# Kernel optimization log

Hardware: AMD Instinct MI355X
Metric: run time of the kernel (lower is better)

The kernel has to match this reference:

```python
import jax, jax.numpy as jnp
import numpy as np

N = 200000
C = 128
VOX = 0.05
EPS = 1e-5
OFFSETS = np.array([[dz, dy, dx] for dz in (-1, 0, 1) for dy in (-1, 0, 1) for dx in (-1, 0, 1)], dtype=np.int64)


def setup_inputs() -> dict:
    key = jax.random.key(0)
    ks = jax.random.split(key, 8)
    gp = jax.random.normal(ks[0], (N, 14), jnp.float32)
    # ---- voxelization tables (int constants, computed once in numpy) ----
    pts = np.asarray(gp[:, :3], dtype=np.float64)
    vc = np.floor(pts / VOX).astype(np.int64)
    vc = vc - vc.min(axis=0)
    mx = vc.max(axis=0) + 1
    h = vc[:, 0] * mx[1] * mx[2] + vc[:, 1] * mx[2] + vc[:, 2]
    uh, inv = np.unique(h, return_inverse=True)
    M = int(uh.shape[0])
    vcoord = np.zeros((M, 3), np.int64)
    vcoord[inv] = vc  # coords identical for same hash
    nbr_idx = np.zeros((M, 27), np.int32)
    nbr_mask = np.zeros((M, 27), np.float32)
    for o in range(27):
        nc = vcoord + OFFSETS[o]
        inb = (nc >= 0).all(1) & (nc < mx).all(1)
        nh = nc[:, 0] * mx[1] * mx[2] + nc[:, 1] * mx[2] + nc[:, 2]
        pos = np.clip(np.searchsorted(uh, nh), 0, M - 1)
        found = inb & (uh[pos] == nh)
        nbr_idx[:, o] = np.where(found, pos, 0)
        nbr_mask[:, o] = found.astype(np.float32)
    s = 0.05
    return {
        'gaussian_params': gp,
        'w_enc': jax.random.normal(ks[1], (14, C), jnp.float32) * s,
        'b_enc': jnp.zeros((C,), jnp.float32),
        'ln_g': jnp.ones((C,), jnp.float32),
        'ln_b': jnp.zeros((C,), jnp.float32),
        'conv_w': jax.random.normal(ks[2], (4, 27, C, C), jnp.float32) * s,
        'bn_g': jnp.ones((4, C), jnp.float32),
        'bn_b': jnp.zeros((4, C), jnp.float32),
        'w1': jax.random.normal(ks[3], (C, C // 2), jnp.float32) * s,
        'b1': jnp.zeros((C // 2,), jnp.float32),
        'w2': jax.random.normal(ks[4], (C // 2, 14), jnp.float32) * s,
        'b2': jnp.zeros((14,), jnp.float32),
        'nbr_mask': jnp.asarray(nbr_mask),
        'inv_idx': jnp.asarray(inv.astype(np.int32)),
        'nbr_idx': jnp.asarray(nbr_idx),
        'num_voxels': M,
    }


def _bn(x, g, b):
    m = x.mean(0)
    v = x.var(0)
    return (x - m) * jax.lax.rsqrt(v + EPS) * g + b


def _subm(x, W, nbr_idx, nbr_mask):
    # submanifold 3x3x3 conv: sum over 27 offsets of masked neighbor gather @ W[o]
    out = jnp.zeros_like(x)
    for o in range(27):
        out = out + (x[nbr_idx[:, o]] * nbr_mask[:, o:o + 1]) @ W[o]
    return out


def _forward(gp, w_enc, b_enc, ln_g, ln_b, conv_w, bn_g, bn_b, w1, b1, w2, b2, nbr_mask, inv_idx, nbr_idx, num_voxels):
    # input encoder: Linear -> LayerNorm -> ReLU
    f = gp @ w_enc + b_enc
    mu = f.mean(-1, keepdims=True)
    var = f.var(-1, keepdims=True)
    f = jax.nn.relu((f - mu) * jax.lax.rsqrt(var + EPS) * ln_g + ln_b)
    # points -> voxels: segment mean (the op the torch code did with a Python loop)
    cnt = jax.ops.segment_sum(jnp.ones((gp.shape[0],), f.dtype), inv_idx, num_segments=num_voxels)
    x = jax.ops.segment_sum(f, inv_idx, num_segments=num_voxels) / cnt[:, None]
    # 2 residual sparse conv blocks (BN uses batch stats, training-mode forward)
    for blk in range(2):
        idn = x
        out = _subm(x, conv_w[2 * blk], nbr_idx, nbr_mask)
        out = jax.nn.relu(_bn(out, bn_g[2 * blk], bn_b[2 * blk]))
        out = _subm(out, conv_w[2 * blk + 1], nbr_idx, nbr_mask)
        x = jax.nn.relu(_bn(out, bn_g[2 * blk + 1], bn_b[2 * blk + 1]) + idn)
    # voxels -> points, output head, residual add
    pf = x[inv_idx]
    delta = jax.nn.relu(pf @ w1 + b1) @ w2 + b2
    return gp[:, :14] + delta


def reference(gaussian_params, w_enc, b_enc, ln_g, ln_b, conv_w, bn_g, bn_b, w1, b1, w2, b2, nbr_mask, inv_idx, nbr_idx, num_voxels):
    return _forward(gaussian_params, w_enc, b_enc, ln_g, ln_b, conv_w, bn_g, bn_b, w1, b1, w2, b2, nbr_mask, inv_idx, nbr_idx, num_voxels)
```

## Files before the change

### kernel.cpp

```cpp
#include <hip/hip_runtime.h>

typedef __bf16 bf16x8 __attribute__((ext_vector_type(8)));
typedef float f32x16 __attribute__((ext_vector_type(16)));

#define LN_EPS 1e-5f

__device__ __forceinline__ unsigned f2bf_rne(float f) {
    unsigned x = __float_as_uint(f);
    return (x + 0x7fffu + ((x >> 16) & 1u)) >> 16;
}

__device__ __forceinline__ float bf2f(unsigned short u) {
    return __uint_as_float((unsigned)u << 16);
}

__global__ void pack_w_kernel(const float* __restrict__ cw, unsigned short* __restrict__ Wp, int E) {
    int idx = blockIdx.x * 256 + threadIdx.x;
    if (idx >= E) return;
    float v = cw[idx];
    int n  = idx & 127;
    int c  = (idx >> 7) & 127;
    int oc = idx >> 14;
    Wp[oc * 16384 + (c >> 3) * 1024 + n * 8 + (c & 7)] = (unsigned short)f2bf_rne(v);
}

__global__ void pack_w1_kernel(const float* __restrict__ w1, unsigned short* __restrict__ Wp1) {
    int idx = blockIdx.x * 256 + threadIdx.x;
    if (idx >= 8192) return;
    int k = idx >> 6, n = idx & 63;
    Wp1[(k >> 3) * 512 + n * 8 + (k & 7)] = (unsigned short)f2bf_rne(w1[k * 64 + n]);
}

__global__ void prep_nbr_kernel(const int* __restrict__ nbr_idx, const float* __restrict__ nbr_mask,
                                int* __restrict__ T, unsigned* __restrict__ act64, int M) {
    int m = blockIdx.x * 256 + threadIdx.x;
    if (m >= M) return;
    unsigned bits = 0;
#pragma unroll
    for (int o = 0; o < 27; ++o) {
        bool f = nbr_mask[m * 27 + o] != 0.f;
        int g = f ? nbr_idx[m * 27 + o] : M;
        T[o * M + m] = g;
        bits |= (f ? 1u : 0u) << o;
    }
    atomicOr(&act64[m >> 6], bits);
}

__global__ __launch_bounds__(256) void encode_kernel(
    const float* __restrict__ gp, const float* __restrict__ w_enc,
    const float* __restrict__ b_enc, const float* __restrict__ ln_g,
    const float* __restrict__ ln_b, const int* __restrict__ inv_idx,
    float* __restrict__ vsum, float* __restrict__ cnt, int N)
{
    int p = blockIdx.x * 4 + (threadIdx.x >> 6);
    int lane = threadIdx.x & 63;
    if (p >= N) return;
    float gv[14];
#pragma unroll
    for (int i = 0; i < 14; ++i) gv[i] = gp[p * 14 + i];
    float f0 = b_enc[lane], f1 = b_enc[lane + 64];
#pragma unroll
    for (int i = 0; i < 14; ++i) {
        f0 = fmaf(gv[i], w_enc[i * 128 + lane], f0);
        f1 = fmaf(gv[i], w_enc[i * 128 + lane + 64], f1);
    }
    float s = f0 + f1;
#pragma unroll
    for (int off = 32; off; off >>= 1) s += __shfl_xor(s, off);
    float mean = s * 0.0078125f;
    float d0 = f0 - mean, d1 = f1 - mean;
    float v = d0 * d0 + d1 * d1;
#pragma unroll
    for (int off = 32; off; off >>= 1) v += __shfl_xor(v, off);
    float rs = rsqrtf(v * 0.0078125f + LN_EPS);
    float h0 = d0 * rs * ln_g[lane] + ln_b[lane];
    float h1 = d1 * rs * ln_g[lane + 64] + ln_b[lane + 64];
    h0 = h0 > 0.f ? h0 : 0.f;
    h1 = h1 > 0.f ? h1 : 0.f;
    int vx = inv_idx[p];
    atomicAdd(&vsum[vx * 128 + lane], h0);
    atomicAdd(&vsum[vx * 128 + lane + 64], h1);
    if (lane == 0) atomicAdd(&cnt[vx], 1.0f);
}

__global__ void vox_mean_kernel(const float* __restrict__ vsum, const float* __restrict__ cnt,
                                unsigned short* __restrict__ out, int total4) {
    int idx = blockIdx.x * 256 + threadIdx.x;
    if (idx >= total4) return;
    int e0 = idx * 4;
    float r = 1.f / cnt[e0 >> 7];
    float4 v = *(const float4*)(vsum + e0);
    uint2 pk;
    pk.x = f2bf_rne(v.x * r) | (f2bf_rne(v.y * r) << 16);
    pk.y = f2bf_rne(v.z * r) | (f2bf_rne(v.w * r) << 16);
    *(uint2*)(out + e0) = pk;
}

__global__ __launch_bounds__(256) void subm_conv_kernel(
    const unsigned short* __restrict__ xin,
    const unsigned short* __restrict__ Wp,
    const int* __restrict__ T, const unsigned* __restrict__ act64,
    float* __restrict__ yout, float* __restrict__ stats, int M)
{
    const int tid = threadIdx.x;
    const int lane = tid & 63;
    const int w = tid >> 6;

    const int nwg = gridDim.x;
    const int orig = blockIdx.x;
    const int xcd = orig & 7;
    const int q8 = nwg >> 3, r8 = nwg & 7;
    const int tile = (xcd < r8 ? xcd * (q8 + 1) : r8 * (q8 + 1) + (xcd - r8) * q8) + (orig >> 3);

    const int m0 = tile * 256;
    const int rw = w * 64;
    const int q = lane >> 5;
    const int l31 = lane & 31;
    int row0 = m0 + rw + l31;
    int row1 = row0 + 32;
    if (row0 >= M) row0 = M - 1;
    if (row1 >= M) row1 = M - 1;

    f32x16 acc0[4], acc1[4];
#pragma unroll
    for (int t = 0; t < 4; ++t)
#pragma unroll
        for (int r = 0; r < 16; ++r) { acc0[t][r] = 0.f; acc1[t][r] = 0.f; }

    const uint4* xin4 = (const uint4*)xin;
    const bf16x8* WpB = (const bf16x8*)Wp;

    unsigned amask = act64[tile * 4 + w];

    if (amask) {
        int o = __ffs(amask) - 1; amask &= amask - 1;
        int h0 = T[o * M + row0], h1 = T[o * M + row1];
        uint4 af0[8], af1[8];
#pragma unroll
        for (int j = 0; j < 8; ++j) {
            af0[j] = xin4[h0 * 16 + 2 * j + q];
            af1[j] = xin4[h1 * 16 + 2 * j + q];
        }
        int o1 = -1;
        if (amask) {
            o1 = __ffs(amask) - 1; amask &= amask - 1;
            h0 = T[o1 * M + row0]; h1 = T[o1 * M + row1];
        }

        while (true) {
            int o2 = -1, i0 = 0, i1 = 0;
            if (amask) {
                o2 = __ffs(amask) - 1; amask &= amask - 1;
                i0 = T[o2 * M + row0]; i1 = T[o2 * M + row1];
            }

            const bf16x8* Bo = WpB + (size_t)o * 2048;
            const bool more = (o1 >= 0);

            __builtin_amdgcn_s_setprio(1);
            bf16x8 bn0 = Bo[q * 128 + l31];
            bf16x8 bn1 = Bo[q * 128 + 32 + l31];
            bf16x8 bn2 = Bo[q * 128 + 64 + l31];
            bf16x8 bn3 = Bo[q * 128 + 96 + l31];
#pragma unroll
            for (int ks = 0; ks < 8; ++ks) {
                bf16x8 bc0 = bn0, bc1 = bn1, bc2 = bn2, bc3 = bn3;
                if (ks < 7) {
                    int kbn = ((ks + 1) << 1) | q;
                    bn0 = Bo[kbn * 128 + l31];
                    bn1 = Bo[kbn * 128 + 32 + l31];
                    bn2 = Bo[kbn * 128 + 64 + l31];
                    bn3 = Bo[kbn * 128 + 96 + l31];
                }
                bf16x8 a0 = *(const bf16x8*)&af0[ks];
                bf16x8 a1 = *(const bf16x8*)&af1[ks];
                if (more) {
                    af0[ks] = xin4[h0 * 16 + 2 * ks + q];
                    af1[ks] = xin4[h1 * 16 + 2 * ks + q];
                }
                acc0[0] = __builtin_amdgcn_mfma_f32_32x32x16_bf16(a0, bc0, acc0[0], 0, 0, 0);
                acc1[0] = __builtin_amdgcn_mfma_f32_32x32x16_bf16(a1, bc0, acc1[0], 0, 0, 0);
                acc0[1] = __builtin_amdgcn_mfma_f32_32x32x16_bf16(a0, bc1, acc0[1], 0, 0, 0);
                acc1[1] = __builtin_amdgcn_mfma_f32_32x32x16_bf16(a1, bc1, acc1[1], 0, 0, 0);
                acc0[2] = __builtin_amdgcn_mfma_f32_32x32x16_bf16(a0, bc2, acc0[2], 0, 0, 0);
                acc1[2] = __builtin_amdgcn_mfma_f32_32x32x16_bf16(a1, bc2, acc1[2], 0, 0, 0);
                acc0[3] = __builtin_amdgcn_mfma_f32_32x32x16_bf16(a0, bc3, acc0[3], 0, 0, 0);
                acc1[3] = __builtin_amdgcn_mfma_f32_32x32x16_bf16(a1, bc3, acc1[3], 0, 0, 0);
            }
            __builtin_amdgcn_s_setprio(0);

            if (!more) break;
            o = o1; o1 = o2; h0 = i0; h1 = i1;
        }
    }

#pragma unroll
    for (int tn = 0; tn < 4; ++tn) {
        int col = tn * 32 + l31;
        float s = 0.f, sq = 0.f;
#pragma unroll
        for (int r = 0; r < 16; ++r) {
            int rloc = (r & 3) + 8 * (r >> 2) + 4 * q + rw;
            int grow = m0 + rloc;
            float v = (grow < M) ? acc0[tn][r] : 0.f;
            if (grow < M) yout[grow * 128 + col] = v;
            s += v; sq += v * v;
        }
#pragma unroll
        for (int r = 0; r < 16; ++r) {
            int rloc = (r & 3) + 8 * (r >> 2) + 4 * q + rw + 32;
            int grow = m0 + rloc;
            float v = (grow < M) ? acc1[tn][r] : 0.f;
            if (grow < M) yout[grow * 128 + col] = v;
            s += v; sq += v * v;
        }
        s += __shfl_xor(s, 32);
        sq += __shfl_xor(sq, 32);
        if (lane < 32) {
            atomicAdd(&stats[col], s);
            atomicAdd(&stats[128 + col], sq);
        }
    }
}

__global__ void bn_relu_kernel(const float* __restrict__ y, const float* __restrict__ stats,
                               const float* __restrict__ g, const float* __restrict__ b,
                               unsigned short* __restrict__ out, int total4, float invM) {
    int idx = blockIdx.x * 256 + threadIdx.x;
    if (idx >= total4) return;
    int e0 = idx * 4;
    int c0 = e0 & 127;
    float4 yv = *(const float4*)(y + e0);
    float h[4];
    const float* yp = (const float*)&yv;
#pragma unroll
    for (int j = 0; j < 4; ++j) {
        int c = c0 + j;
        float mean = stats[c] * invM;
        float var = stats[128 + c] * invM - mean * mean;
        float sc = g[c] * rsqrtf(var + LN_EPS);
        float sh = b[c] - mean * sc;
        float vv = yp[j] * sc + sh;
        h[j] = vv > 0.f ? vv : 0.f;
    }
    uint2 pk;
    pk.x = f2bf_rne(h[0]) | (f2bf_rne(h[1]) << 16);
    pk.y = f2bf_rne(h[2]) | (f2bf_rne(h[3]) << 16);
    *(uint2*)(out + e0) = pk;
}

__global__ void bn_relu_res_kernel(const float* __restrict__ y, const float* __restrict__ stats,
                                   const float* __restrict__ g, const float* __restrict__ b,
                                   const unsigned short* __restrict__ idn,
                                   unsigned short* __restrict__ out, int total4, float invM) {
    int idx = blockIdx.x * 256 + threadIdx.x;
    if (idx >= total4) return;
    int e0 = idx * 4;
    int c0 = e0 & 127;
    float4 yv = *(const float4*)(y + e0);
    uint2 iv = *(const uint2*)(idn + e0);
    float id[4];
    id[0] = __uint_as_float(iv.x << 16);
    id[1] = __uint_as_float(iv.x & 0xffff0000u);
    id[2] = __uint_as_float(iv.y << 16);
    id[3] = __uint_as_float(iv.y & 0xffff0000u);
    float h[4];
    const float* yp = (const float*)&yv;
#pragma unroll
    for (int j = 0; j < 4; ++j) {
        int c = c0 + j;
        float mean = stats[c] * invM;
        float var = stats[128 + c] * invM - mean * mean;
        float sc = g[c] * rsqrtf(var + LN_EPS);
        float sh = b[c] - mean * sc;
        float vv = yp[j] * sc + sh + id[j];
        h[j] = vv > 0.f ? vv : 0.f;
    }
    uint2 pk;
    pk.x = f2bf_rne(h[0]) | (f2bf_rne(h[1]) << 16);
    pk.y = f2bf_rne(h[2]) | (f2bf_rne(h[3]) << 16);
    *(uint2*)(out + e0) = pk;
}

__global__ __launch_bounds__(256) void head_vox_kernel(
    const unsigned short* __restrict__ A,
    const unsigned short* __restrict__ Wp1,
    const float* __restrict__ b1, const float* __restrict__ w2,
    const float* __restrict__ b2, float* __restrict__ Dv, int M)
{
    __shared__ uint4 W1s[1024];
    __shared__ unsigned short Hs[8192];
    __shared__ float w2s[896];

    const int tid = threadIdx.x;
    const int lane = tid & 63;
    const int w = tid >> 6;
    const int m0 = blockIdx.x * 128;
    const int rw = w * 32;
    const int q = lane >> 5;
    const int l31 = lane & 31;
    int myrow = m0 + rw + l31;
    if (myrow > M) myrow = M;

    for (int i = tid; i < 1024; i += 256) W1s[i] = ((const uint4*)Wp1)[i];
    for (int i = tid; i < 896; i += 256) w2s[i] = w2[i];

    const uint4* xin4 = (const uint4*)A;
    uint4 af[8];
#pragma unroll
    for (int j = 0; j < 8; ++j) af[j] = xin4[myrow * 16 + 2 * j + q];

    f32x16 acc[2];
#pragma unroll
    for (int t = 0; t < 2; ++t)
#pragma unroll
        for (int r = 0; r < 16; ++r) acc[t][r] = 0.f;

    __syncthreads();

#pragma unroll
    for (int ks = 0; ks < 8; ++ks) {
        int kb = (ks << 1) | q;
        bf16x8 a = *(const bf16x8*)&af[ks];
#pragma unroll
        for (int tn = 0; tn < 2; ++tn) {
            bf16x8 b = ((const bf16x8*)W1s)[kb * 64 + tn * 32 + l31];
            acc[tn] = __builtin_amdgcn_mfma_f32_32x32x16_bf16(a, b, acc[tn], 0, 0, 0);
        }
    }

#pragma unroll
    for (int tn = 0; tn < 2; ++tn) {
        int col = tn * 32 + l31;
        float bias = b1[col];
        int ch = col >> 3, ce = col & 7;
#pragma unroll
        for (int r = 0; r < 16; ++r) {
            int rloc = (r & 3) + 8 * (r >> 2) + 4 * q + rw;
            float v = acc[tn][r] + bias;
            v = v > 0.f ? v : 0.f;
            Hs[rloc * 64 + (ch ^ (rloc & 7)) * 8 + ce] = (unsigned short)f2bf_rne(v);
        }
    }
    __syncthreads();

    int r2 = tid >> 1;
    int c0 = (tid & 1) * 7;
    float o[7];
#pragma unroll
    for (int j = 0; j < 7; ++j) o[j] = b2[c0 + j];
#pragma unroll
    for (int c = 0; c < 8; ++c) {
        bf16x8 hv = ((const bf16x8*)Hs)[r2 * 8 + (c ^ (r2 & 7))];
#pragma unroll
        for (int e = 0; e < 8; ++e) {
            float h = bf2f(((const unsigned short*)&hv)[e]);
            int k = c * 8 + e;
#pragma unroll
            for (int j = 0; j < 7; ++j) o[j] = fmaf(h, w2s[k * 14 + c0 + j], o[j]);
        }
    }
    int grow = m0 + r2;
    if (grow < M) {
#pragma unroll
        for (int j = 0; j < 7; ++j) Dv[grow * 14 + c0 + j] = o[j];
    }
}

__global__ void head_scatter_kernel(const float* __restrict__ gp, const float* __restrict__ Dv,
                                    const int* __restrict__ inv_idx, float* __restrict__ out, int N) {
    int p = blockIdx.x * 256 + threadIdx.x;
    if (p >= N) return;
    int vx = inv_idx[p];
#pragma unroll
    for (int c = 0; c < 14; ++c) out[p * 14 + c] = gp[p * 14 + c] + Dv[vx * 14 + c];
}

extern "C" void kernel_launch(void* const* d_in, const int* in_sizes, int n_in,
                              void* d_out, int out_size, void* d_ws, size_t ws_size,
                              hipStream_t stream) {
    const float* gp       = (const float*)d_in[0];
    const float* w_enc    = (const float*)d_in[1];
    const float* b_enc    = (const float*)d_in[2];
    const float* ln_g     = (const float*)d_in[3];
    const float* ln_b     = (const float*)d_in[4];
    const float* conv_w   = (const float*)d_in[5];
    const float* bn_g     = (const float*)d_in[6];
    const float* bn_b     = (const float*)d_in[7];
    const float* w1       = (const float*)d_in[8];
    const float* b1       = (const float*)d_in[9];
    const float* w2       = (const float*)d_in[10];
    const float* b2       = (const float*)d_in[11];
    const float* nbr_mask = (const float*)d_in[12];
    const int*   inv_idx  = (const int*)d_in[13];
    const int*   nbr_idx  = (const int*)d_in[14];

    const int N = in_sizes[0] / 14;
    const int M = in_sizes[12] / 27;
    const int ntiles = (M + 127) / 128;
    const int ntiles256 = (M + 255) / 256;

    char* ws = (char*)d_ws;
    size_t off = 0;
    unsigned short* Wp = (unsigned short*)(ws + off); off += (size_t)4 * 27 * 16384 * 2;
    unsigned short* A  = (unsigned short*)(ws + off); off += (size_t)(M + 1) * 128 * 2;
    unsigned short* H  = (unsigned short*)(ws + off); off += (size_t)(M + 1) * 128 * 2;
    float* Yraw  = (float*)(ws + off);
    size_t zoff = off;
    off += (size_t)M * 128 * 4;
    float* cnt   = (float*)(ws + off); off += (size_t)M * 4;
    float* stats = (float*)(ws + off); off += 4 * 256 * 4;
    unsigned* act64 = (unsigned*)(ws + off); off += (size_t)ntiles256 * 4 * 4;
    size_t zbytes = off - zoff;
    int* T = (int*)(ws + off); off += (size_t)27 * M * 4;
    unsigned short* Wp1 = (unsigned short*)(ws + off); off += 8192 * 2;
    float* Dv = Yraw;

    hipMemsetAsync(Yraw, 0, zbytes, stream);
    hipMemsetAsync(A + (size_t)M * 128, 0, 256, stream);
    hipMemsetAsync(H + (size_t)M * 128, 0, 256, stream);

    const int E = 4 * 27 * 128 * 128;
    pack_w_kernel<<<(E + 255) / 256, 256, 0, stream>>>(conv_w, Wp, E);
    pack_w1_kernel<<<32, 256, 0, stream>>>(w1, Wp1);
    prep_nbr_kernel<<<(M + 255) / 256, 256, 0, stream>>>(nbr_idx, nbr_mask, T, act64, M);
    encode_kernel<<<(N + 3) / 4, 256, 0, stream>>>(gp, w_enc, b_enc, ln_g, ln_b, inv_idx, Yraw, cnt, N);
    const int total4 = M * 32;
    vox_mean_kernel<<<(total4 + 255) / 256, 256, 0, stream>>>(Yraw, cnt, A, total4);

    const float invM = 1.f / (float)M;
    for (int blk = 0; blk < 2; ++blk) {
        int c0 = 2 * blk, c1 = 2 * blk + 1;
        subm_conv_kernel<<<ntiles256, 256, 0, stream>>>(
            A, Wp + (size_t)c0 * 27 * 16384, T, act64, Yraw, stats + c0 * 256, M);
        bn_relu_kernel<<<(total4 + 255) / 256, 256, 0, stream>>>(
            Yraw, stats + c0 * 256, bn_g + c0 * 128, bn_b + c0 * 128, H, total4, invM);
        subm_conv_kernel<<<ntiles256, 256, 0, stream>>>(
            H, Wp + (size_t)c1 * 27 * 16384, T, act64, Yraw, stats + c1 * 256, M);
        bn_relu_res_kernel<<<(total4 + 255) / 256, 256, 0, stream>>>(
            Yraw, stats + c1 * 256, bn_g + c1 * 128, bn_b + c1 * 128, A, A, total4, invM);
    }
    head_vox_kernel<<<ntiles, 256, 0, stream>>>(A, Wp1, b1, w2, b2, Dv, M);
    head_scatter_kernel<<<(N + 255) / 256, 256, 0, stream>>>(gp, Dv, inv_idx, (float*)d_out, N);
}
```

Before: 1.424 ms.

## Split first sparse conv into 256-row and 128-row tile launches

Adds a 128-row-tile variant of the submanifold conv kernel with one accumulator set per wave. It splits only the first conv of block 0: half the 256-row tiles run in the original kernel and the remaining rows in the new smaller-tile kernel. The aim is better load balance and occupancy on the tail, with XCD-aware tile remapping. It adds an extra launch, and applying it to a single conv looks experimental and asymmetric.

After: 1.530 ms. 7.5% more time.

```diff
diff --git a/kernel.cpp b/kernel.cpp
--- a/kernel.cpp
+++ b/kernel.cpp
@@ -223,6 +223,99 @@
     }
 }
 
+__global__ __launch_bounds__(256) void subm_conv32_kernel(
+    const unsigned short* __restrict__ xin,
+    const unsigned short* __restrict__ Wp,
+    const int* __restrict__ T, const unsigned* __restrict__ act64,
+    float* __restrict__ yout, float* __restrict__ stats, int M, int base)
+{
+    const int tid = threadIdx.x;
+    const int lane = tid & 63;
+    const int w = tid >> 6;
+
+    const int nwg = gridDim.x;
+    const int orig = blockIdx.x;
+    const int xcd = orig & 7;
+    const int q8 = nwg >> 3, r8 = nwg & 7;
+    const int tile = (xcd < r8 ? xcd * (q8 + 1) : r8 * (q8 + 1) + (xcd - r8) * q8) + (orig >> 3);
+
+    const int m0 = base + tile * 128;
+    const int rw = w * 32;
+    const int q = lane >> 5;
+    const int l31 = lane & 31;
+    int row0 = m0 + rw + l31;
+    if (row0 >= M) row0 = M - 1;
+
+    f32x16 acc0[4];
+#pragma unroll
+    for (int t = 0; t < 4; ++t)
+#pragma unroll
+        for (int r = 0; r < 16; ++r) acc0[t][r] = 0.f;
+
+    const uint4* xin4 = (const uint4*)xin;
+    const bf16x8* WpB = (const bf16x8*)Wp;
+
+    unsigned amask = act64[(m0 >> 6) + (w >> 1)];
+
+    if (amask) {
+        int o = __ffs(amask) - 1; amask &= amask - 1;
+        int h0 = T[o * M + row0];
+        uint4 af0[8];
+#pragma unroll
+        for (int j = 0; j < 8; ++j) af0[j] = xin4[h0 * 16 + 2 * j + q];
+        int o1 = -1;
+        if (amask) { o1 = __ffs(amask) - 1; amask &= amask - 1; h0 = T[o1 * M + row0]; }
+
+        while (true) {
+            int o2 = -1, i0 = 0;
+            if (amask) { o2 = __ffs(amask) - 1; amask &= amask - 1; i0 = T[o2 * M + row0]; }
+
+            const bf16x8* Bo = WpB + (size_t)o * 2048;
+            const bool more = (o1 >= 0);
+
+            __builtin_amdgcn_s_setprio(1);
+#pragma unroll
+            for (int ks = 0; ks < 8; ++ks) {
+                int kb = (ks << 1) | q;
+                bf16x8 b0 = Bo[kb * 128 + l31];
+                bf16x8 b1 = Bo[kb * 128 + 32 + l31];
+                bf16x8 b2 = Bo[kb * 128 + 64 + l31];
+                bf16x8 b3 = Bo[kb * 128 + 96 + l31];
+                bf16x8 a0 = *(const bf16x8*)&af0[ks];
+                if (more) af0[ks] = xin4[h0 * 16 + 2 * ks + q];
+                acc0[0] = __builtin_amdgcn_mfma_f32_32x32x16_bf16(a0, b0, acc0[0], 0, 0, 0);
+                acc0[1] = __builtin_amdgcn_mfma_f32_32x32x16_bf16(a0, b1, acc0[1], 0, 0, 0);
+                acc0[2] = __builtin_amdgcn_mfma_f32_32x32x16_bf16(a0, b2, acc0[2], 0, 0, 0);
+                acc0[3] = __builtin_amdgcn_mfma_f32_32x32x16_bf16(a0, b3, acc0[3], 0, 0, 0);
+            }
+            __builtin_amdgcn_s_setprio(0);
+
+            if (!more) break;
+            o = o1; o1 = o2; h0 = i0;
+        }
+    }
+
+#pragma unroll
+    for (int tn = 0; tn < 4; ++tn) {
+        int col = tn * 32 + l31;
+        float s = 0.f, sq = 0.f;
+#pragma unroll
+        for (int r = 0; r < 16; ++r) {
+            int rloc = (r & 3) + 8 * (r >> 2) + 4 * q + rw;
+            int grow = m0 + rloc;
+            float v = (grow < M) ? acc0[tn][r] : 0.f;
+            if (grow < M) yout[grow * 128 + col] = v;
+            s += v; sq += v * v;
+        }
+        s += __shfl_xor(s, 32);
+        sq += __shfl_xor(sq, 32);
+        if (lane < 32) {
+            atomicAdd(&stats[col], s);
+            atomicAdd(&stats[128 + col], sq);
+        }
+    }
+}
+
 __global__ void bn_relu_kernel(const float* __restrict__ y, const float* __restrict__ stats,
                                const float* __restrict__ g, const float* __restrict__ b,
                                unsigned short* __restrict__ out, int total4, float invM) {
@@ -400,6 +493,10 @@
     const int ntiles = (M + 127) / 128;
     const int ntiles256 = (M + 255) / 256;
 
+    const int ntilesA = ntiles256 / 2;
+    const int rA = ntilesA * 256;
+    const int ntilesB = (M - rA + 127) / 128;
+
     char* ws = (char*)d_ws;
     size_t off = 0;
     unsigned short* Wp = (unsigned short*)(ws + off); off += (size_t)4 * 27 * 16384 * 2;
@@ -431,8 +528,15 @@
     const float invM = 1.f / (float)M;
     for (int blk = 0; blk < 2; ++blk) {
         int c0 = 2 * blk, c1 = 2 * blk + 1;
-        subm_conv_kernel<<<ntiles256, 256, 0, stream>>>(
-            A, Wp + (size_t)c0 * 27 * 16384, T, act64, Yraw, stats + c0 * 256, M);
+        if (blk == 0 && ntilesA > 0 && ntilesB > 0) {
+            subm_conv_kernel<<<ntilesA, 256, 0, stream>>>(
+                A, Wp + (size_t)c0 * 27 * 16384, T, act64, Yraw, stats + c0 * 256, M);
+            subm_conv32_kernel<<<ntilesB, 256, 0, stream>>>(
+                A, Wp + (size_t)c0 * 27 * 16384, T, act64, Yraw, stats + c0 * 256, M, rA);
+        } else {
+            subm_conv_kernel<<<ntiles256, 256, 0, stream>>>(
+                A, Wp + (size_t)c0 * 27 * 16384, T, act64, Yraw, stats + c0 * 256, M);
+        }
         bn_relu_kernel<<<(total4 + 255) / 256, 256, 0, stream>>>(
             Yraw, stats + c0 * 256, bn_g + c0 * 128, bn_b + c0 * 128, H, total4, invM);
         subm_conv_kernel<<<ntiles256, 256, 0, stream>>>(
```

## Double rows per wave in sparse conv to reuse weight fragments

Applied to the files above, without the earlier changes.

Each wave of the submanifold conv kernel now computes 128 rows instead of 64, so one weight-fragment load feeds four MFMA row blocks instead of two. Tiles grow to 512 rows and the per-wave active-offset mask becomes the OR of two 64-row group masks. Weight prefetch moves to two k-steps ahead. This cuts weight-load traffic per MFMA but roughly doubles accumulator and A-fragment register use, forcing one block per CU (launch_bounds 256,1). It also halves the grid and adds wasted work on offsets that are active in only one of the two groups.

New measurement: 1.456 ms. 1.02x slower.

```diff
diff --git a/kernel.cpp b/kernel.cpp
--- a/kernel.cpp
+++ b/kernel.cpp
@@ -96,7 +96,7 @@
     *(uint2*)(out + e0) = pk;
 }
 
-__global__ __launch_bounds__(256) void subm_conv_kernel(
+__global__ __launch_bounds__(256, 1) void subm_conv_kernel(
     const unsigned short* __restrict__ xin,
     const unsigned short* __restrict__ Wp,
     const int* __restrict__ T, const unsigned* __restrict__ act64,
@@ -112,46 +112,58 @@
     const int q8 = nwg >> 3, r8 = nwg & 7;
     const int tile = (xcd < r8 ? xcd * (q8 + 1) : r8 * (q8 + 1) + (xcd - r8) * q8) + (orig >> 3);
 
-    const int m0 = tile * 256;
-    const int rw = w * 64;
+    const int m0 = tile * 512;
+    const int rw = w * 128;
     const int q = lane >> 5;
     const int l31 = lane & 31;
     int row0 = m0 + rw + l31;
     int row1 = row0 + 32;
+    int row2 = row0 + 64;
+    int row3 = row0 + 96;
     if (row0 >= M) row0 = M - 1;
     if (row1 >= M) row1 = M - 1;
-
-    f32x16 acc0[4], acc1[4];
+    if (row2 >= M) row2 = M - 1;
+    if (row3 >= M) row3 = M - 1;
+
+    f32x16 acc0[4], acc1[4], acc2[4], acc3[4];
 #pragma unroll
     for (int t = 0; t < 4; ++t)
 #pragma unroll
-        for (int r = 0; r < 16; ++r) { acc0[t][r] = 0.f; acc1[t][r] = 0.f; }
+        for (int r = 0; r < 16; ++r) {
+            acc0[t][r] = 0.f; acc1[t][r] = 0.f; acc2[t][r] = 0.f; acc3[t][r] = 0.f;
+        }
 
     const uint4* xin4 = (const uint4*)xin;
     const bf16x8* WpB = (const bf16x8*)Wp;
 
-    unsigned amask = act64[tile * 4 + w];
+    const int g64 = (m0 + rw) >> 6;
+    unsigned amask = act64[g64] | act64[g64 + 1];
 
     if (amask) {
         int o = __ffs(amask) - 1; amask &= amask - 1;
         int h0 = T[o * M + row0], h1 = T[o * M + row1];
-        uint4 af0[8], af1[8];
+        int h2 = T[o * M + row2], h3 = T[o * M + row3];
+        uint4 af0[8], af1[8], af2[8], af3[8];
 #pragma unroll
         for (int j = 0; j < 8; ++j) {
             af0[j] = xin4[h0 * 16 + 2 * j + q];
             af1[j] = xin4[h1 * 16 + 2 * j + q];
+            af2[j] = xin4[h2 * 16 + 2 * j + q];
+            af3[j] = xin4[h3 * 16 + 2 * j + q];
         }
         int o1 = -1;
         if (amask) {
             o1 = __ffs(amask) - 1; amask &= amask - 1;
             h0 = T[o1 * M + row0]; h1 = T[o1 * M + row1];
+            h2 = T[o1 * M + row2]; h3 = T[o1 * M + row3];
         }
 
         while (true) {
-            int o2 = -1, i0 = 0, i1 = 0;
+            int o2 = -1, i0 = 0, i1 = 0, i2 = 0, i3 = 0;
             if (amask) {
                 o2 = __ffs(amask) - 1; amask &= amask - 1;
                 i0 = T[o2 * M + row0]; i1 = T[o2 * M + row1];
+                i2 = T[o2 * M + row2]; i3 = T[o2 * M + row3];
             }
 
             const bf16x8* Bo = WpB + (size_t)o * 2048;
@@ -162,35 +174,53 @@
             bf16x8 bn1 = Bo[q * 128 + 32 + l31];
             bf16x8 bn2 = Bo[q * 128 + 64 + l31];
             bf16x8 bn3 = Bo[q * 128 + 96 + l31];
+            bf16x8 bm0 = Bo[(2 | q) * 128 + l31];
+            bf16x8 bm1 = Bo[(2 | q) * 128 + 32 + l31];
+            bf16x8 bm2 = Bo[(2 | q) * 128 + 64 + l31];
+            bf16x8 bm3 = Bo[(2 | q) * 128 + 96 + l31];
 #pragma unroll
             for (int ks = 0; ks < 8; ++ks) {
                 bf16x8 bc0 = bn0, bc1 = bn1, bc2 = bn2, bc3 = bn3;
-                if (ks < 7) {
-                    int kbn = ((ks + 1) << 1) | q;
-                    bn0 = Bo[kbn * 128 + l31];
-                    bn1 = Bo[kbn * 128 + 32 + l31];
-                    bn2 = Bo[kbn * 128 + 64 + l31];
-                    bn3 = Bo[kbn * 128 + 96 + l31];
+                bn0 = bm0; bn1 = bm1; bn2 = bm2; bn3 = bm3;
+                if (ks < 6) {
+                    int kbn = ((ks + 2) << 1) | q;
+                    bm0 = Bo[kbn * 128 + l31];
+                    bm1 = Bo[kbn * 128 + 32 + l31];
+                    bm2 = Bo[kbn * 128 + 64 + l31];
+                    bm3 = Bo[kbn * 128 + 96 + l31];
                 }
                 bf16x8 a0 = *(const bf16x8*)&af0[ks];
                 bf16x8 a1 = *(const bf16x8*)&af1[ks];
+                bf16x8 a2 = *(const bf16x8*)&af2[ks];
+                bf16x8 a3 = *(const bf16x8*)&af3[ks];
                 if (more) {
                     af0[ks] = xin4[h0 * 16 + 2 * ks + q];
                     af1[ks] = xin4[h1 * 16 + 2 * ks + q];
+                    af2[ks] = xin4[h2 * 16 + 2 * ks + q];
+                    af3[ks] = xin4[h3 * 16 + 2 * ks + q];
                 }
                 acc0[0] = __builtin_amdgcn_mfma_f32_32x32x16_bf16(a0, bc0, acc0[0], 0, 0, 0);
                 acc1[0] = __builtin_amdgcn_mfma_f32_32x32x16_bf16(a1, bc0, acc1[0], 0, 0, 0);
+                acc2[0] = __builtin_amdgcn_mfma_f32_32x32x16_bf16(a2, bc0, acc2[0], 0, 0, 0);
+                acc3[0] = __builtin_amdgcn_mfma_f32_32x32x16_bf16(a3, bc0, acc3[0], 0, 0, 0);
                 acc0[1] = __builtin_amdgcn_mfma_f32_32x32x16_bf16(a0, bc1, acc0[1], 0, 0, 0);
                 acc1[1] = __builtin_amdgcn_mfma_f32_32x32x16_bf16(a1, bc1, acc1[1], 0, 0, 0);
+                acc2[1] = __builtin_amdgcn_mfma_f32_32x32x16_bf16(a2, bc1, acc2[1], 0, 0, 0);
+                acc3[1] = __builtin_amdgcn_mfma_f32_32x32x16_bf16(a3, bc1, acc3[1], 0, 0, 0);
                 acc0[2] = __builtin_amdgcn_mfma_f32_32x32x16_bf16(a0, bc2, acc0[2], 0, 0, 0);
                 acc1[2] = __builtin_amdgcn_mfma_f32_32x32x16_bf16(a1, bc2, acc1[2], 0, 0, 0);
+                acc2[2] = __builtin_amdgcn_mfma_f32_32x32x16_bf16(a2, bc2, acc2[2], 0, 0, 0);
+                acc3[2] = __builtin_amdgcn_mfma_f32_32x32x16_bf16(a3, bc2, acc3[2], 0, 0, 0);
                 acc0[3] = __builtin_amdgcn_mfma_f32_32x32x16_bf16(a0, bc3, acc0[3], 0, 0, 0);
                 acc1[3] = __builtin_amdgcn_mfma_f32_32x32x16_bf16(a1, bc3, acc1[3], 0, 0, 0);
+                acc2[3] = __builtin_amdgcn_mfma_f32_32x32x16_bf16(a2, bc3, acc2[3], 0, 0, 0);
+                acc3[3] = __builtin_amdgcn_mfma_f32_32x32x16_bf16(a3, bc3, acc3[3], 0, 0, 0);
             }
             __builtin_amdgcn_s_setprio(0);
 
             if (!more) break;
-            o = o1; o1 = o2; h0 = i0; h1 = i1;
+            o = o1; o1 = o2;
+            h0 = i0; h1 = i1; h2 = i2; h3 = i3;
         }
     }
 
@@ -199,20 +229,20 @@
         int col = tn * 32 + l31;
         float s = 0.f, sq = 0.f;
 #pragma unroll
-        for (int r = 0; r < 16; ++r) {
-            int rloc = (r & 3) + 8 * (r >> 2) + 4 * q + rw;
-            int grow = m0 + rloc;
-            float v = (grow < M) ? acc0[tn][r] : 0.f;
-            if (grow < M) yout[grow * 128 + col] = v;
-            s += v; sq += v * v;
-        }
-#pragma unroll
-        for (int r = 0; r < 16; ++r) {
-            int rloc = (r & 3) + 8 * (r >> 2) + 4 * q + rw + 32;
-            int grow = m0 + rloc;
-            float v = (grow < M) ? acc1[tn][r] : 0.f;
-            if (grow < M) yout[grow * 128 + col] = v;
-            s += v; sq += v * v;
+        for (int rb = 0; rb < 4; ++rb) {
+#pragma unroll
+            for (int r = 0; r < 16; ++r) {
+                int rloc = (r & 3) + 8 * (r >> 2) + 4 * q + rw + rb * 32;
+                int grow = m0 + rloc;
+                float v;
+                if (rb == 0) v = acc0[tn][r];
+                else if (rb == 1) v = acc1[tn][r];
+                else if (rb == 2) v = acc2[tn][r];
+                else v = acc3[tn][r];
+                v = (grow < M) ? v : 0.f;
+                if (grow < M) yout[grow * 128 + col] = v;
+                s += v; sq += v * v;
+            }
         }
         s += __shfl_xor(s, 32);
         sq += __shfl_xor(sq, 32);
@@ -398,7 +428,8 @@
     const int N = in_sizes[0] / 14;
     const int M = in_sizes[12] / 27;
     const int ntiles = (M + 127) / 128;
-    const int ntiles256 = (M + 255) / 256;
+    const int ntiles512 = (M + 511) / 512;
+    const int ngroups64 = (M + 63) / 64;
 
     char* ws = (char*)d_ws;
     size_t off = 0;
@@ -410,11 +441,12 @@
     off += (size_t)M * 128 * 4;
     float* cnt   = (float*)(ws + off); off += (size_t)M * 4;
     float* stats = (float*)(ws + off); off += 4 * 256 * 4;
-    unsigned* act64 = (unsigned*)(ws + off); off += (size_t)ntiles256 * 4 * 4;
+    unsigned* act64 = (unsigned*)(ws + off); off += (size_t)(ntiles512 * 8 + 8) * 4;
     size_t zbytes = off - zoff;
     int* T = (int*)(ws + off); off += (size_t)27 * M * 4;
     unsigned short* Wp1 = (unsigned short*)(ws + off); off += 8192 * 2;
     float* Dv = Yraw;
+    (void)ngroups64;
 
     hipMemsetAsync(Yraw, 0, zbytes, stream);
     hipMemsetAsync(A + (size_t)M * 128, 0, 256, stream);
@@ -431,11 +463,11 @@
     const float invM = 1.f / (float)M;
     for (int blk = 0; blk < 2; ++blk) {
         int c0 = 2 * blk, c1 = 2 * blk + 1;
-        subm_conv_kernel<<<ntiles256, 256, 0, stream>>>(
+        subm_conv_kernel<<<ntiles512, 256, 0, stream>>>(
             A, Wp + (size_t)c0 * 27 * 16384, T, act64, Yraw, stats + c0 * 256, M);
         bn_relu_kernel<<<(total4 + 255) / 256, 256, 0, stream>>>(
             Yraw, stats + c0 * 256, bn_g + c0 * 128, bn_b + c0 * 128, H, total4, invM);
-        subm_conv_kernel<<<ntiles256, 256, 0, stream>>>(
+        subm_conv_kernel<<<ntiles512, 256, 0, stream>>>(
             H, Wp + (size_t)c1 * 27 * 16384, T, act64, Yraw, stats + c1 * 256, M);
         bn_relu_res_kernel<<<(total4 + 255) / 256, 256, 0, stream>>>(
             Yraw, stats + c1 * 256, bn_g + c1 * 128, bn_b + c1 * 128, A, A, total4, invM);
```
